# Optimization experiments

Measured on AMD Instinct MI355X. Metric: run time of the kernel, lower is better.

The kernel has to match this reference:

```python
import jax, jax.numpy as jnp
import numpy as np

DIM, N_HEAD, DK, DV = 1024, 16, 64, 64
B, S = 1, 4096


def setup_inputs() -> dict:
    key = jax.random.key(0)
    ks = jax.random.split(key, 9)
    sd = 0.02
    return {
        "x": jax.random.normal(ks[0], (B, S, DIM), dtype=jnp.float32),
        "Wq": jax.random.normal(ks[1], (DIM, N_HEAD * DK), dtype=jnp.float32) * sd,
        "bq": jnp.zeros((N_HEAD * DK,), dtype=jnp.float32),
        "Wk": jax.random.normal(ks[2], (DIM, N_HEAD * DK), dtype=jnp.float32) * sd,
        "bk": jnp.zeros((N_HEAD * DK,), dtype=jnp.float32),
        "Wv": jax.random.normal(ks[3], (DIM, N_HEAD * DV), dtype=jnp.float32) * sd,
        "bv": jnp.zeros((N_HEAD * DV,), dtype=jnp.float32),
        "Wo": jax.random.normal(ks[4], (N_HEAD * DV, DIM), dtype=jnp.float32) * sd,
        "bo": jnp.zeros((DIM,), dtype=jnp.float32),
    }


def reference(x, Wq, bq, Wk, bk, Wv, bv, Wo, bo):
    b, s, _ = x.shape
    scale = DK ** (-0.5)
    # projections -> [b, h, s, d]
    q = (x @ Wq + bq).reshape(b, s, N_HEAD, DK).transpose(0, 2, 1, 3)
    k = (x @ Wk + bk).reshape(b, s, N_HEAD, DK).transpose(0, 2, 1, 3)
    v = (x @ Wv + bv).reshape(b, s, N_HEAD, DV).transpose(0, 2, 1, 3)
    attn = jnp.einsum("bhqd,bhkd->bhqk", q, k) * scale  # [b,h,s,s]
    attn = jax.nn.softmax(attn, axis=-1)
    out = jnp.einsum("bhqk,bhkd->bhqd", attn, v)  # [b,h,s,dv]
    out = out.transpose(0, 2, 1, 3).reshape(b, s, N_HEAD * DV)
    return out @ Wo + bo
```

## Files before the change

### kernel.cpp

```cpp
#include <hip/hip_runtime.h>
#include <hip/hip_bf16.h>
#include <hip/hip_fp16.h>

#define SEQ 4096
#define DIM 1024
#define NH 16
#define NT (SEQ / 64)

typedef __attribute__((ext_vector_type(4))) float f32x4;
typedef __attribute__((ext_vector_type(8))) _Float16 half8;
typedef __attribute__((ext_vector_type(4))) _Float16 half4;
typedef __attribute__((ext_vector_type(2))) unsigned uint2v;

#if __has_builtin(__builtin_amdgcn_exp2f)
#define EXP2(x) __builtin_amdgcn_exp2f(x)
#else
#define EXP2(x) exp2f(x)
#endif

#define SMC 0.18033688f


__global__ __launch_bounds__(256) void conv_x(const float* __restrict__ x,
                                              _Float16* __restrict__ xh, int n) {
  int i = (blockIdx.x * 256 + threadIdx.x) * 4;
  if (i >= n) return;
  float4 v = *reinterpret_cast<const float4*>(x + i);
  half4 h;
  h[0] = (_Float16)v.x; h[1] = (_Float16)v.y;
  h[2] = (_Float16)v.z; h[3] = (_Float16)v.w;
  *reinterpret_cast<half4*>(xh + i) = h;
}

__global__ __launch_bounds__(256) void conv_wT4(const float* __restrict__ W0,
                                                const float* __restrict__ W1,
                                                const float* __restrict__ W2,
                                                const float* __restrict__ W3,
                                                _Float16* __restrict__ T0,
                                                _Float16* __restrict__ T1,
                                                _Float16* __restrict__ T2,
                                                _Float16* __restrict__ T3) {
  const float* W = blockIdx.z == 0 ? W0 : blockIdx.z == 1 ? W1 : blockIdx.z == 2 ? W2 : W3;
  _Float16* Wt = blockIdx.z == 0 ? T0 : blockIdx.z == 1 ? T1 : blockIdx.z == 2 ? T2 : T3;
  __shared__ float t[32][33];
  int bx = blockIdx.x * 32;
  int by = blockIdx.y * 32;
  int tx = threadIdx.x & 31, ty = threadIdx.x >> 5;
#pragma unroll
  for (int i = 0; i < 4; i++)
    t[ty + i * 8][tx] = W[(by + ty + i * 8) * DIM + bx + tx];
  __syncthreads();
#pragma unroll
  for (int i = 0; i < 4; i++)
    Wt[(bx + ty + i * 8) * DIM + by + tx] = (_Float16)t[tx][ty + i * 8];
}

template <int MODE>
__device__ __forceinline__ void gemm_body(const _Float16* __restrict__ A,
                                          const _Float16* __restrict__ Bt,
                                          const float* __restrict__ bias,
                                          void* __restrict__ outp,
                                          int M, int N, int Kd, int bmb, int bnb) {
  __shared__ __align__(16) _Float16 As[64][72];
  __shared__ __align__(16) _Float16 Bs[128][72];
  const int tid = threadIdx.x, lane = tid & 63, w = tid >> 6;
  const int bm = bmb * 64, bn = bnb * 128;
  const int l15 = lane & 15, g = lane >> 4, kb = g * 8;
  const int sra = tid >> 2, sca = (tid & 3) * 16;
  const int srb = tid >> 1, scb = (tid & 1) * 32;
  f32x4 acc[4][2] = {};

  uint4 ar0, ar1, br0, br1, br2, br3;
  auto LOADT = [&](int k0) {
    const _Float16* ap = A + (size_t)(bm + sra) * Kd + k0 + sca;
    ar0 = *reinterpret_cast<const uint4*>(ap);
    ar1 = *reinterpret_cast<const uint4*>(ap + 8);
    const _Float16* bp = Bt + (size_t)(bn + srb) * Kd + k0 + scb;
    br0 = *reinterpret_cast<const uint4*>(bp);
    br1 = *reinterpret_cast<const uint4*>(bp + 8);
    br2 = *reinterpret_cast<const uint4*>(bp + 16);
    br3 = *reinterpret_cast<const uint4*>(bp + 24);
  };

  LOADT(0);
  for (int k0 = 0; k0 < Kd; k0 += 64) {
    __syncthreads();
    *reinterpret_cast<uint4*>(&As[sra][sca]) = ar0;
    *reinterpret_cast<uint4*>(&As[sra][sca + 8]) = ar1;
    *reinterpret_cast<uint4*>(&Bs[srb][scb]) = br0;
    *reinterpret_cast<uint4*>(&Bs[srb][scb + 8]) = br1;
    *reinterpret_cast<uint4*>(&Bs[srb][scb + 16]) = br2;
    *reinterpret_cast<uint4*>(&Bs[srb][scb + 24]) = br3;
    __syncthreads();
    if (k0 + 64 < Kd) LOADT(k0 + 64);
#pragma unroll
    for (int kk = 0; kk < 64; kk += 32) {
      half8 af[4], bf[2];
#pragma unroll
      for (int i = 0; i < 4; i++)
        af[i] = *reinterpret_cast<const half8*>(&As[i * 16 + l15][kk + kb]);
#pragma unroll
      for (int j = 0; j < 2; j++)
        bf[j] = *reinterpret_cast<const half8*>(&Bs[w * 32 + j * 16 + l15][kk + kb]);
      __builtin_amdgcn_s_setprio(1);
#pragma unroll
      for (int i = 0; i < 4; i++)
#pragma unroll
        for (int j = 0; j < 2; j++)
          acc[i][j] = __builtin_amdgcn_mfma_f32_16x16x32_f16(af[i], bf[j], acc[i][j], 0, 0, 0);
      __builtin_amdgcn_s_setprio(0);
    }
  }

#pragma unroll
  for (int i = 0; i < 4; i++)
#pragma unroll
    for (int j = 0; j < 2; j++) {
      const int row0 = bm + i * 16 + g * 4;
      const int col = bn + w * 32 + j * 16 + l15;
      if (MODE == 2) {
        half4 hv;
#pragma unroll
        for (int r = 0; r < 4; r++) hv[r] = (_Float16)(acc[i][j][r] + bias[col]);
        *reinterpret_cast<half4*>(&((_Float16*)outp)[(size_t)col * M + row0]) = hv;
      } else {
#pragma unroll
        for (int r = 0; r < 4; r++) {
          float vv = acc[i][j][r] + bias[col];
          if (MODE == 0) {
            _Float16* O = (_Float16*)outp;
            O[(((col >> 6) * SEQ) + row0 + r) * 64 + (col & 63)] = (_Float16)vv;
          } else {
            float* O = (float*)outp;
            O[(size_t)(row0 + r) * N + col] = vv;
          }
        }
      }
    }
}

__global__ __launch_bounds__(256) void gemm_qkv(const _Float16* __restrict__ A,
                                                const _Float16* __restrict__ WqT,
                                                const _Float16* __restrict__ WkT,
                                                const _Float16* __restrict__ WvT,
                                                const float* __restrict__ bq,
                                                const float* __restrict__ bk,
                                                const float* __restrict__ bv,
                                                _Float16* __restrict__ Qd,
                                                _Float16* __restrict__ Kd,
                                                _Float16* __restrict__ Vd) {
  if (blockIdx.z == 0)
    gemm_body<0>(A, WqT, bq, (void*)Qd, SEQ, DIM, DIM, blockIdx.x, blockIdx.y);
  else if (blockIdx.z == 1)
    gemm_body<0>(A, WkT, bk, (void*)Kd, SEQ, DIM, DIM, blockIdx.x, blockIdx.y);
  else
    gemm_body<2>(A, WvT, bv, (void*)Vd, SEQ, DIM, DIM, blockIdx.x, blockIdx.y);
}

__global__ __launch_bounds__(256) void gemm_out(const _Float16* __restrict__ A,
                                                const _Float16* __restrict__ Bt,
                                                const float* __restrict__ bias,
                                                float* __restrict__ out) {
  gemm_body<1>(A, Bt, bias, (void*)out, SEQ, DIM, DIM, blockIdx.x, blockIdx.y);
}

__global__ __launch_bounds__(256) void attn_fwd(const _Float16* __restrict__ Q,
                                                const _Float16* __restrict__ Kh,
                                                const _Float16* __restrict__ Vt_g,
                                                _Float16* __restrict__ Og) {
  __shared__ __align__(16) _Float16 Ks[3][64][72];
  __shared__ __align__(16) _Float16 Vs[3][64][72];
  __shared__ __align__(16) _Float16 Ps[4][2][16][72];
  const int h = blockIdx.y;
  const int q0 = blockIdx.x * 128;
  const int tid = threadIdx.x, lane = tid & 63, w = tid >> 6;
  const int l15 = lane & 15, g = lane >> 4, kb = g * 8;

  const int qrow = q0 + w * 32 + l15;
  const _Float16* qp = Q + ((size_t)h * SEQ + qrow) * 64;
  half8 qf[2][2];
  qf[0][0] = *reinterpret_cast<const half8*>(qp + kb);
  qf[0][1] = *reinterpret_cast<const half8*>(qp + 32 + kb);
  qf[1][0] = *reinterpret_cast<const half8*>(qp + 16 * 64 + kb);
  qf[1][1] = *reinterpret_cast<const half8*>(qp + 16 * 64 + 32 + kb);

  f32x4 o[2][4] = {};
  f32x4 ol[2] = {};
  float m[2] = {-1e30f, -1e30f};
  float negmC[2] = {1e30f, 1e30f};

  const f32x4 kZero = {0.f, 0.f, 0.f, 0.f};
  const _Float16 one1 = (_Float16)1.f;
  const half8 kOnes8 = {one1, one1, one1, one1, one1, one1, one1, one1};

  const int srow = tid >> 3, sc8 = (tid & 7) * 8;
  const _Float16* kbase = Kh + (size_t)h * SEQ * 64;
  const _Float16* vbase = Vt_g + (size_t)h * 64 * SEQ;

  uint4 kr0, kr1, vr0, vr1;
  auto LOADKV = [&](int kt2) {
    const _Float16* kp = kbase + (size_t)(kt2 * 64 + srow) * 64 + sc8;
    kr0 = *reinterpret_cast<const uint4*>(kp);
    kr1 = *reinterpret_cast<const uint4*>(kp + 32 * 64);
    const _Float16* vp = vbase + (size_t)srow * SEQ + kt2 * 64 + sc8;
    vr0 = *reinterpret_cast<const uint4*>(vp);
    vr1 = *reinterpret_cast<const uint4*>(vp + 32 * SEQ);
  };
  auto STAGE = [&](int buf) {
    *reinterpret_cast<uint4*>(&Ks[buf][srow][sc8]) = kr0;
    *reinterpret_cast<uint4*>(&Ks[buf][srow + 32][sc8]) = kr1;
    *reinterpret_cast<uint4*>(&Vs[buf][srow][sc8]) = vr0;
    *reinterpret_cast<uint4*>(&Vs[buf][srow + 32][sc8]) = vr1;
  };

  auto QK = [&](int tile, f32x4 (&sf)[2][4]) {
    const int b = tile % 3;
    __builtin_amdgcn_s_setprio(1);
#pragma unroll
    for (int f = 0; f < 4; f++) {
      half8 kf0 = *reinterpret_cast<const half8*>(&Ks[b][f * 16 + l15][kb]);
      half8 kf1 = *reinterpret_cast<const half8*>(&Ks[b][f * 16 + l15][32 + kb]);
      sf[0][f] = __builtin_amdgcn_mfma_f32_16x16x32_f16(kf0, qf[0][0], kZero, 0, 0, 0);
      sf[0][f] = __builtin_amdgcn_mfma_f32_16x16x32_f16(kf1, qf[0][1], sf[0][f], 0, 0, 0);
      sf[1][f] = __builtin_amdgcn_mfma_f32_16x16x32_f16(kf0, qf[1][0], kZero, 0, 0, 0);
      sf[1][f] = __builtin_amdgcn_mfma_f32_16x16x32_f16(kf1, qf[1][1], sf[1][f], 0, 0, 0);
    }
    __builtin_amdgcn_s_setprio(0);
  };

  auto ITER = [&](int t, f32x4 (&scur)[2][4], f32x4 (&snext)[2][4]) {
    if (t + 1 < NT) QK(t + 1, snext);

#pragma unroll
    for (int s = 0; s < 2; s++) {
      float m0 = fmaxf(fmaxf(scur[s][0][0], scur[s][0][1]), scur[s][0][2]);
      float m1 = fmaxf(fmaxf(scur[s][0][3], scur[s][1][0]), scur[s][1][1]);
      float m2 = fmaxf(fmaxf(scur[s][1][2], scur[s][1][3]), scur[s][2][0]);
      float m3 = fmaxf(fmaxf(scur[s][2][1], scur[s][2][2]), scur[s][2][3]);
      float m4 = fmaxf(fmaxf(scur[s][3][0], scur[s][3][1]), scur[s][3][2]);
      float pm = fmaxf(fmaxf(fmaxf(m0, m1), m2), fmaxf(fmaxf(m3, m4), scur[s][3][3]));
      if (__any(pm > m[s] + 64.f)) {
        pm = fmaxf(pm, __shfl_xor(pm, 16, 64));
        pm = fmaxf(pm, __shfl_xor(pm, 32, 64));
        float mn = fmaxf(m[s], pm);
        float al = EXP2((m[s] - mn) * SMC);
        m[s] = mn;
        negmC[s] = -mn * SMC;
        ol[s] *= al;
#pragma unroll
        for (int f = 0; f < 4; f++) o[s][f] *= al;
      }
#pragma unroll
      for (int f = 0; f < 4; f++) {
        float p0 = EXP2(fmaf(scur[s][f][0], SMC, negmC[s]));
        float p1 = EXP2(fmaf(scur[s][f][1], SMC, negmC[s]));
        float p2 = EXP2(fmaf(scur[s][f][2], SMC, negmC[s]));
        float p3 = EXP2(fmaf(scur[s][f][3], SMC, negmC[s]));
        auto h01 = __builtin_amdgcn_cvt_pkrtz(p0, p1);
        auto h23 = __builtin_amdgcn_cvt_pkrtz(p2, p3);
        uint2v uu = {__builtin_bit_cast(unsigned, h01), __builtin_bit_cast(unsigned, h23)};
        *reinterpret_cast<half4*>(&Ps[w][s][l15][f * 16 + g * 4]) =
            __builtin_bit_cast(half4, uu);
      }
    }

    half8 pa[2][2];
#pragma unroll
    for (int s = 0; s < 2; s++) {
      pa[s][0] = *reinterpret_cast<const half8*>(&Ps[w][s][l15][kb]);
      pa[s][1] = *reinterpret_cast<const half8*>(&Ps[w][s][l15][32 + kb]);
    }

    const int bv = t % 3;
    __builtin_amdgcn_s_setprio(1);
#pragma unroll
    for (int f = 0; f < 4; f++) {
      half8 vf0 = *reinterpret_cast<const half8*>(&Vs[bv][f * 16 + l15][kb]);
      half8 vf1 = *reinterpret_cast<const half8*>(&Vs[bv][f * 16 + l15][32 + kb]);
      o[0][f] = __builtin_amdgcn_mfma_f32_16x16x32_f16(vf0, pa[0][0], o[0][f], 0, 0, 0);
      o[0][f] = __builtin_amdgcn_mfma_f32_16x16x32_f16(vf1, pa[0][1], o[0][f], 0, 0, 0);
      o[1][f] = __builtin_amdgcn_mfma_f32_16x16x32_f16(vf0, pa[1][0], o[1][f], 0, 0, 0);
      o[1][f] = __builtin_amdgcn_mfma_f32_16x16x32_f16(vf1, pa[1][1], o[1][f], 0, 0, 0);
    }
    ol[0] = __builtin_amdgcn_mfma_f32_16x16x32_f16(kOnes8, pa[0][0], ol[0], 0, 0, 0);
    ol[0] = __builtin_amdgcn_mfma_f32_16x16x32_f16(kOnes8, pa[0][1], ol[0], 0, 0, 0);
    ol[1] = __builtin_amdgcn_mfma_f32_16x16x32_f16(kOnes8, pa[1][0], ol[1], 0, 0, 0);
    ol[1] = __builtin_amdgcn_mfma_f32_16x16x32_f16(kOnes8, pa[1][1], ol[1], 0, 0, 0);
    __builtin_amdgcn_s_setprio(0);

    if (t + 2 < NT) STAGE((t + 2) % 3);
    if (t + 3 < NT) LOADKV(t + 3);
    __syncthreads();
  };

  LOADKV(0); STAGE(0);
  LOADKV(1); STAGE(1);
  LOADKV(2);
  __syncthreads();

  f32x4 sfA[2][4], sfB[2][4];
  QK(0, sfA);
  for (int t = 0; t < NT; t += 2) {
    ITER(t, sfA, sfB);
    ITER(t + 1, sfB, sfA);
  }

#pragma unroll
  for (int s = 0; s < 2; s++) {
    float rinv = 1.f / ol[s][0];
#pragma unroll
    for (int f = 0; f < 4; f++) {
      half4 hv;
#pragma unroll
      for (int r = 0; r < 4; r++) hv[r] = (_Float16)(o[s][f][r] * rinv);
      *reinterpret_cast<half4*>(
          &Og[(size_t)(qrow + 16 * s) * DIM + h * 64 + f * 16 + g * 4]) = hv;
    }
  }
}


extern "C" void kernel_launch(void* const* d_in, const int* in_sizes, int n_in,
                              void* d_out, int out_size, void* d_ws, size_t ws_size,
                              hipStream_t stream) {
  const float* x  = (const float*)d_in[0];
  const float* Wq = (const float*)d_in[1];
  const float* bq = (const float*)d_in[2];
  const float* Wk = (const float*)d_in[3];
  const float* bk = (const float*)d_in[4];
  const float* Wv = (const float*)d_in[5];
  const float* bv = (const float*)d_in[6];
  const float* Wo = (const float*)d_in[7];
  const float* bo = (const float*)d_in[8];

  char* ws = (char*)d_ws;
  _Float16* xh  = (_Float16*)ws;
  _Float16* WqT = (_Float16*)(ws + (size_t)SEQ * DIM * 2);
  _Float16* WkT = WqT + DIM * DIM;
  _Float16* WvT = WkT + DIM * DIM;
  _Float16* WoT = WvT + DIM * DIM;
  _Float16* Qd  = WoT + DIM * DIM;
  _Float16* Kd  = Qd + (size_t)SEQ * DIM;
  _Float16* Vd  = Kd + (size_t)SEQ * DIM;
  _Float16* Od  = Vd + (size_t)SEQ * DIM;

  conv_x<<<(SEQ * DIM) / 1024, 256, 0, stream>>>(x, xh, SEQ * DIM);
  conv_wT4<<<dim3(32, 32, 4), 256, 0, stream>>>(Wq, Wk, Wv, Wo, WqT, WkT, WvT, WoT);

  gemm_qkv<<<dim3(SEQ / 64, DIM / 128, 3), 256, 0, stream>>>(
      xh, WqT, WkT, WvT, bq, bk, bv, Qd, Kd, Vd);

  attn_fwd<<<dim3(SEQ / 128, NH), 256, 0, stream>>>(Qd, Kd, Vd, Od);

  gemm_out<<<dim3(SEQ / 64, DIM / 128), 256, 0, stream>>>(Od, WoT, bo, (float*)d_out);
}
```

Baseline: 177.0 us.

## Merge prep kernels and permute V/P key ordering for vectorized LDS stores

Fuses the x fp16 conversion and the weight transpose kernels into one launch using an extra grid z-slice, removing one kernel launch. The V-transpose epilogue now writes rows in a permuted order (g*16+i*4), which lets the attention kernel store each lane's softmax probabilities as two contiguous 16-byte LDS writes instead of four 8-byte writes. The permutation must stay consistent between V's key ordering and P's column ordering for correctness.

New measurement: 176.1 us. Within noise of the previous version (-0.5%).

```diff
diff --git a/kernel.cpp b/kernel.cpp
--- a/kernel.cpp
+++ b/kernel.cpp
@@ -20,19 +20,9 @@
 
 #define SMC 0.18033688f
 
-
-__global__ __launch_bounds__(256) void conv_x(const float* __restrict__ x,
-                                              _Float16* __restrict__ xh, int n) {
-  int i = (blockIdx.x * 256 + threadIdx.x) * 4;
-  if (i >= n) return;
-  float4 v = *reinterpret_cast<const float4*>(x + i);
-  half4 h;
-  h[0] = (_Float16)v.x; h[1] = (_Float16)v.y;
-  h[2] = (_Float16)v.z; h[3] = (_Float16)v.w;
-  *reinterpret_cast<half4*>(xh + i) = h;
-}
-
-__global__ __launch_bounds__(256) void conv_wT4(const float* __restrict__ W0,
+__global__ __launch_bounds__(256) void prep_all(const float* __restrict__ x,
+                                                _Float16* __restrict__ xh,
+                                                const float* __restrict__ W0,
                                                 const float* __restrict__ W1,
                                                 const float* __restrict__ W2,
                                                 const float* __restrict__ W3,
@@ -40,6 +30,19 @@
                                                 _Float16* __restrict__ T1,
                                                 _Float16* __restrict__ T2,
                                                 _Float16* __restrict__ T3) {
+  if (blockIdx.z == 4) {
+    const int blkid = blockIdx.x * 32 + blockIdx.y;
+#pragma unroll
+    for (int u = 0; u < 4; u++) {
+      int i = blkid * 4096 + u * 1024 + threadIdx.x * 4;
+      float4 v = *reinterpret_cast<const float4*>(x + i);
+      half4 h;
+      h[0] = (_Float16)v.x; h[1] = (_Float16)v.y;
+      h[2] = (_Float16)v.z; h[3] = (_Float16)v.w;
+      *reinterpret_cast<half4*>(xh + i) = h;
+    }
+    return;
+  }
   const float* W = blockIdx.z == 0 ? W0 : blockIdx.z == 1 ? W1 : blockIdx.z == 2 ? W2 : W3;
   _Float16* Wt = blockIdx.z == 0 ? T0 : blockIdx.z == 1 ? T1 : blockIdx.z == 2 ? T2 : T3;
   __shared__ float t[32][33];
@@ -116,14 +119,15 @@
   for (int i = 0; i < 4; i++)
 #pragma unroll
     for (int j = 0; j < 2; j++) {
-      const int row0 = bm + i * 16 + g * 4;
       const int col = bn + w * 32 + j * 16 + l15;
       if (MODE == 2) {
+        const int rowP = bm + g * 16 + i * 4;
         half4 hv;
 #pragma unroll
         for (int r = 0; r < 4; r++) hv[r] = (_Float16)(acc[i][j][r] + bias[col]);
-        *reinterpret_cast<half4*>(&((_Float16*)outp)[(size_t)col * M + row0]) = hv;
+        *reinterpret_cast<half4*>(&((_Float16*)outp)[(size_t)col * M + rowP]) = hv;
       } else {
+        const int row0 = bm + i * 16 + g * 4;
 #pragma unroll
         for (int r = 0; r < 4; r++) {
           float vv = acc[i][j][r] + bias[col];
@@ -250,18 +254,20 @@
 #pragma unroll
         for (int f = 0; f < 4; f++) o[s][f] *= al;
       }
+      unsigned us[8];
 #pragma unroll
       for (int f = 0; f < 4; f++) {
         float p0 = EXP2(fmaf(scur[s][f][0], SMC, negmC[s]));
         float p1 = EXP2(fmaf(scur[s][f][1], SMC, negmC[s]));
         float p2 = EXP2(fmaf(scur[s][f][2], SMC, negmC[s]));
         float p3 = EXP2(fmaf(scur[s][f][3], SMC, negmC[s]));
-        auto h01 = __builtin_amdgcn_cvt_pkrtz(p0, p1);
-        auto h23 = __builtin_amdgcn_cvt_pkrtz(p2, p3);
-        uint2v uu = {__builtin_bit_cast(unsigned, h01), __builtin_bit_cast(unsigned, h23)};
-        *reinterpret_cast<half4*>(&Ps[w][s][l15][f * 16 + g * 4]) =
-            __builtin_bit_cast(half4, uu);
+        us[2 * f] = __builtin_bit_cast(unsigned, __builtin_amdgcn_cvt_pkrtz(p0, p1));
+        us[2 * f + 1] = __builtin_bit_cast(unsigned, __builtin_amdgcn_cvt_pkrtz(p2, p3));
       }
+      uint4 w0 = {us[0], us[1], us[2], us[3]};
+      uint4 w1 = {us[4], us[5], us[6], us[7]};
+      *reinterpret_cast<uint4*>(&Ps[w][s][l15][g * 16]) = w0;
+      *reinterpret_cast<uint4*>(&Ps[w][s][l15][g * 16 + 8]) = w1;
     }
 
     half8 pa[2][2];
@@ -344,8 +350,8 @@
   _Float16* Vd  = Kd + (size_t)SEQ * DIM;
   _Float16* Od  = Vd + (size_t)SEQ * DIM;
 
-  conv_x<<<(SEQ * DIM) / 1024, 256, 0, stream>>>(x, xh, SEQ * DIM);
-  conv_wT4<<<dim3(32, 32, 4), 256, 0, stream>>>(Wq, Wk, Wv, Wo, WqT, WkT, WvT, WoT);
+  prep_all<<<dim3(32, 32, 5), 256, 0, stream>>>(x, xh, Wq, Wk, Wv, Wo,
+                                                WqT, WkT, WvT, WoT);
 
   gemm_qkv<<<dim3(SEQ / 64, DIM / 128, 3), 256, 0, stream>>>(
       xh, WqT, WkT, WvT, bq, bk, bv, Qd, Kd, Vd);
```
